# Optimization experiments

Hardware: AMD Instinct MI355X
Metric: run time of the kernel (lower is better)

## Reference

```python
import jax, jax.numpy as jnp
import numpy as np

D_MODEL = 2048
N_HEADS = 32
N_KV = 8
HEAD_DIM = D_MODEL // N_HEADS  # 64
ROPE_BASE = 500000.0


def _rope_tables(seq_len, dim, dtype):
    inv_freq = 1.0 / (ROPE_BASE ** (jnp.arange(0, dim, 2, dtype=jnp.float32) / dim))
    t = jnp.arange(seq_len, dtype=jnp.float32)
    freqs = jnp.outer(t, inv_freq)          # [S, dim/2]
    emb = jnp.concatenate([freqs, freqs], axis=-1)  # [S, dim]
    return jnp.cos(emb).astype(dtype), jnp.sin(emb).astype(dtype)


def _rotate_half(x):
    x1, x2 = jnp.split(x, 2, axis=-1)
    return jnp.concatenate([-x2, x1], axis=-1)


def setup_inputs() -> dict:
    key = jax.random.key(0)
    ks = jax.random.split(key, 5)
    B, S = 2, 2048
    sc = 0.02
    return {
        "x": jax.random.normal(ks[0], (B, S, D_MODEL), jnp.float32),
        "Wq": jax.random.normal(ks[1], (D_MODEL, N_HEADS * HEAD_DIM), jnp.float32) * sc,
        "Wk": jax.random.normal(ks[2], (D_MODEL, N_KV * HEAD_DIM), jnp.float32) * sc,
        "Wv": jax.random.normal(ks[3], (D_MODEL, N_KV * HEAD_DIM), jnp.float32) * sc,
        "Wo": jax.random.normal(ks[4], (N_HEADS * HEAD_DIM, D_MODEL), jnp.float32) * sc,
    }


def reference(x, Wq, Wk, Wv, Wo):
    B, S, _ = x.shape
    n_rep = N_HEADS // N_KV

    q = (x @ Wq).reshape(B, S, N_HEADS, HEAD_DIM)
    k = (x @ Wk).reshape(B, S, N_KV, HEAD_DIM)
    v = (x @ Wv).reshape(B, S, N_KV, HEAD_DIM)

    cos, sin = _rope_tables(S, HEAD_DIM, x.dtype)
    cos = cos[None, :, None, :]  # [1,S,1,D]
    sin = sin[None, :, None, :]
    q = q * cos + _rotate_half(q) * sin
    k = k * cos + _rotate_half(k) * sin

    # GQA without materializing expanded K/V: group q heads by kv head.
    qg = q.reshape(B, S, N_KV, n_rep, HEAD_DIM)
    scale = 1.0 / jnp.sqrt(jnp.asarray(HEAD_DIM, x.dtype))
    # scores: [B, n_kv, n_rep, Sq, Sk]
    scores = jnp.einsum("bqhrd,bkhd->bhrqk", qg, k) * scale
    attn = jax.nn.softmax(scores, axis=-1)
    out = jnp.einsum("bhrqk,bkhd->bqhrd", attn, v)  # [B,S,n_kv,n_rep,D]
    out = out.reshape(B, S, N_HEADS * HEAD_DIM)
    return out @ Wo
```

## Files before the change

kernel.cpp:

```cpp
#include <hip/hip_runtime.h>
#include <hip/hip_bf16.h>
#include <stdint.h>

#define SS    2048
#define BB    2
#define MT    4096
#define DM    2048
#define NQKVC 3072

typedef __attribute__((ext_vector_type(8))) short s16x8;
typedef __attribute__((ext_vector_type(4))) short s16x4;
typedef __attribute__((ext_vector_type(4))) float f32x4;
typedef __attribute__((ext_vector_type(2))) unsigned u32x2;

typedef __attribute__((address_space(1))) const void* as1cv;
typedef __attribute__((address_space(3))) void* as3v;

__device__ __forceinline__ float b2f(int u) {
  union { unsigned u; float f; } x; x.u = ((unsigned)(u & 0xFFFF)) << 16; return x.f;
}
__device__ __forceinline__ short f2b(float f) {
  union { float f; unsigned u; } x; x.f = f;
  unsigned r = x.u + 0x7FFFu + ((x.u >> 16) & 1u);
  return (short)(r >> 16);
}
__device__ __forceinline__ void gld16(const void* g, void* l) {
  __builtin_amdgcn_global_load_lds((as1cv)(uintptr_t)g, (as3v)(uint32_t)(uintptr_t)l, 16, 0, 0);
}
__device__ __forceinline__ s16x8 ldsfrag(const char* tile, int r, int cb) {
  return *(const s16x8*)(tile + r * 128 + (cb ^ ((r & 7) << 4)));
}
__device__ __forceinline__ f32x4 mfma16(s16x8 a, s16x8 b, f32x4 c) {
  return __builtin_amdgcn_mfma_f32_16x16x32_bf16(a, b, c, 0, 0, 0);
}
__device__ __forceinline__ void swz8(int& bx, int& by) {
  int gx = gridDim.x;
  int lin = by * gx + bx;
  int tot = gx * gridDim.y;
  int s = (lin & 7) * (tot >> 3) + (lin >> 3);
  bx = s % gx;
  by = s / gx;
}

__global__ __launch_bounds__(256) void k_wpre(const float* __restrict__ x,
                                              const float* __restrict__ Wq,
                                              const float* __restrict__ Wk,
                                              const float* __restrict__ Wv,
                                              const float* __restrict__ Wo,
                                              ushort* __restrict__ xb,
                                              ushort* __restrict__ Wqkvt,
                                              ushort* __restrict__ Wot,
                                              float* __restrict__ rtab) {
  __shared__ float t[32][33];
  int bid = blockIdx.x;
  if (bid < 8192) {
    int i = (bid * 256 + threadIdx.x) * 4;
    float4 v = *(const float4*)(x + i);
    s16x4 o = { f2b(v.x), f2b(v.y), f2b(v.z), f2b(v.w) };
    *(s16x4*)(xb + i) = o;
    return;
  }
  bid -= 8192;
  if (bid >= 10240) {
    int idx = (bid - 10240) * 256 + threadIdx.x;
    int d = idx & 31, s = idx >> 5;
    float invf = exp2f(-(float)d * (18.931568569324174f / 32.0f));
    float sn, c;
    sincosf((float)s * invf, &sn, &c);
    rtab[idx * 2]     = c;
    rtab[idx * 2 + 1] = sn;
    return;
  }
  const float* W; ushort* out; int N; int l;
  if (bid < 4096)      { W = Wq; out = Wqkvt;                         N = 2048; l = bid; }
  else if (bid < 5120) { W = Wk; out = Wqkvt + (size_t)2048 * 2048;   N = 512;  l = bid - 4096; }
  else if (bid < 6144) { W = Wv; out = Wqkvt + (size_t)2560 * 2048;   N = 512;  l = bid - 5120; }
  else                 { W = Wo; out = Wot;                           N = 2048; l = bid - 6144; }
  int k0 = (l & 63) * 32, n0 = (l >> 6) * 32;
  int tx = threadIdx.x & 31, ty = threadIdx.x >> 5;
#pragma unroll
  for (int j = 0; j < 32; j += 8)
    t[ty + j][tx] = W[(size_t)(k0 + ty + j) * N + n0 + tx];
  __syncthreads();
  int tx2 = threadIdx.x & 15, rr = threadIdx.x >> 4;
#pragma unroll
  for (int j = 0; j < 32; j += 16) {
    int nl = rr + j;
    ushort2 w;
    w.x = (ushort)f2b(t[tx2 * 2][nl]);
    w.y = (ushort)f2b(t[tx2 * 2 + 1][nl]);
    *(ushort2*)(out + (size_t)(n0 + nl) * 2048 + k0 + tx2 * 2) = w;
  }
}

template <int BF16_OUT, int ROPE>
__global__ __launch_bounds__(256) void k_gemm(const ushort* __restrict__ A,
                                              const ushort* __restrict__ B,
                                              void* __restrict__ Cv,
                                              const float* __restrict__ rtab,
                                              ushort* __restrict__ Vt,
                                              int M, int N, int K) {
  __shared__ __align__(16) char lds[32768];
  char* ldsA = lds;
  char* ldsB = lds + 16384;
  int bx = blockIdx.x, by = blockIdx.y;
  swz8(bx, by);
  int tid = threadIdx.x, lane = tid & 63, wid = tid >> 6;
  int wr = wid >> 1, wc = wid & 1;
  int row0 = by * 128, col0 = bx * 128;
  int fr = lane & 15, fq = lane >> 4;
  f32x4 acc[4][4] = {};
  int rl = lane >> 3;
  int cbs = ((lane & 7) << 4) ^ (rl << 4);
  const char* Ab = (const char*)A;
  const char* Bb = (const char*)B;
  size_t ldb = (size_t)K * 2;

  for (int kt = 0; kt < K; kt += 64) {
#pragma unroll
    for (int i = 0; i < 4; i++) {
      int ra = wid * 32 + i * 8 + rl;
      gld16(Ab + (size_t)(row0 + ra) * ldb + (size_t)kt * 2 + cbs,
            ldsA + (wid * 32 + i * 8) * 128);
      gld16(Bb + (size_t)(col0 + ra) * ldb + (size_t)kt * 2 + cbs,
            ldsB + (wid * 32 + i * 8) * 128);
    }
    __syncthreads();
#pragma unroll
    for (int kk = 0; kk < 2; kk++) {
      int cb = kk * 64 + (fq << 4);
      s16x8 af[4], bg[4];
#pragma unroll
      for (int m = 0; m < 4; m++) af[m] = ldsfrag(ldsA, wr * 64 + m * 16 + fr, cb);
#pragma unroll
      for (int n = 0; n < 4; n++) bg[n] = ldsfrag(ldsB, wc * 64 + n * 16 + fr, cb);
#pragma unroll
      for (int m = 0; m < 4; m++)
#pragma unroll
        for (int n = 0; n < 4; n++)
          acc[m][n] = mfma16(af[m], bg[n], acc[m][n]);
    }
    __syncthreads();
  }

  int cb0 = col0 + wc * 64;

  if (ROPE && col0 >= 2560) {
    __syncthreads();
    char* tw = lds + wid * 8192;
#pragma unroll
    for (int m = 0; m < 4; m++)
#pragma unroll
      for (int n = 0; n < 4; n++) {
        int cl = n * 16 + fr;
        unsigned u01, u23;
        asm("v_cvt_pk_bf16_f32 %0, %1, %2" : "=v"(u01) : "v"(acc[m][n][0]), "v"(acc[m][n][1]));
        asm("v_cvt_pk_bf16_f32 %0, %1, %2" : "=v"(u23) : "v"(acc[m][n][2]), "v"(acc[m][n][3]));
        u32x2 w = {u01, u23};
        *(u32x2*)(tw + cl * 128 + (((m * 16 + fq * 4) * 2) ^ ((cl & 7) << 4))) = w;
      }
    asm volatile("" ::: "memory");
    int b = row0 >> 11;
    int s0 = row0 - b * 2048 + wr * 64;
    int vrow0 = b * 512 + (cb0 - 2560);
#pragma unroll
    for (int jj = 0; jj < 8; jj++) {
      int cl = jj * 8 + (lane >> 3);
      int ch = lane & 7;
      s16x8 v = *(const s16x8*)(tw + cl * 128 + ((ch * 16) ^ ((cl & 7) << 4)));
      *(s16x8*)(Vt + (size_t)(vrow0 + cl) * SS + s0 + ch * 8) = v;
    }
    return;
  }

  if (ROPE) {
    if (cb0 < 2560) {
      float qs = (cb0 < 2048) ? 0.18033688011112042f : 1.0f;
#pragma unroll
      for (int m = 0; m < 4; m++)
#pragma unroll
        for (int i = 0; i < 4; i++) {
          int srow = (row0 + wr * 64 + m * 16 + fq * 4 + i) & (SS - 1);
          const float* tr = rtab + srow * 64;
          float cs0 = tr[fr * 2],        sn0 = tr[fr * 2 + 1];
          float cs1 = tr[32 + fr * 2],   sn1 = tr[32 + fr * 2 + 1];
          float lo0 = acc[m][0][i], hi0 = acc[m][2][i];
          acc[m][0][i] = (lo0 * cs0 - hi0 * sn0) * qs;
          acc[m][2][i] = (hi0 * cs0 + lo0 * sn0) * qs;
          float lo1 = acc[m][1][i], hi1 = acc[m][3][i];
          acc[m][1][i] = (lo1 * cs1 - hi1 * sn1) * qs;
          acc[m][3][i] = (hi1 * cs1 + lo1 * sn1) * qs;
        }
    }
  }

#pragma unroll
  for (int m = 0; m < 4; m++) {
#pragma unroll
    for (int i = 0; i < 4; i++) {
      int row = row0 + wr * 64 + m * 16 + fq * 4 + i;
      if (BF16_OUT) {
        ushort* C = (ushort*)Cv;
#pragma unroll
        for (int n = 0; n < 4; n++)
          C[(size_t)row * N + col0 + wc * 64 + n * 16 + fr] = (ushort)f2b(acc[m][n][i]);
      } else {
        float* C = (float*)Cv;
#pragma unroll
        for (int n = 0; n < 4; n++)
          C[(size_t)row * N + col0 + wc * 64 + n * 16 + fr] = acc[m][n][i];
      }
    }
  }
}

__global__ __launch_bounds__(256) void k_attn(const ushort* __restrict__ QKV,
                                              const ushort* __restrict__ Vt,
                                              ushort* __restrict__ O) {
  __shared__ __align__(16) char ldsK[16384];
  __shared__ __align__(16) char ldsV[16384];
  __shared__ __align__(16) char ldsP[4][2048];
  int bx = blockIdx.x, by = blockIdx.y;
  swz8(bx, by);
  int tid = threadIdx.x, lane = tid & 63, wid = tid >> 6;
  int bh = by, b = bh >> 5, h = bh & 31, kv = h >> 2;
  int fr = lane & 15, fq = lane >> 4;
  int q0 = bx * 128 + wid * 32;

  s16x8 qf[2][2];
#pragma unroll
  for (int kk = 0; kk < 2; kk++)
#pragma unroll
    for (int qi = 0; qi < 2; qi++)
      qf[kk][qi] = *(const s16x8*)(QKV + (size_t)(b * SS + q0 + qi * 16 + fr) * NQKVC
                                   + h * 64 + kk * 32 + fq * 8);

  const f32x4 fz = {0.f, 0.f, 0.f, 0.f};
  f32x4 o[4][2];
  f32x4 psum[2] = {fz, fz};
#pragma unroll
  for (int n = 0; n < 4; n++) { o[n][0] = fz; o[n][1] = fz; }
  const short ONE = 0x3F80;
  const s16x8 ones = {ONE, ONE, ONE, ONE, ONE, ONE, ONE, ONE};

  int rl = lane >> 3;
  int cbs = ((lane & 7) << 4) ^ (rl << 4);
  const char* Kbase = (const char*)QKV + (size_t)(b * SS) * (NQKVC * 2) + (size_t)(2048 + kv * 64) * 2;
  const char* Vbase = (const char*)Vt + (size_t)((b * 8 + kv) * 64) * (SS * 2);
  char* pw = ldsP[wid];
  int pswz = (fr & 7) << 4;

  for (int t = 0; t < SS / 128; t++) {
#pragma unroll
    for (int j = 0; j < 4; j++) {
      int rr = wid * 32 + j * 8;
      gld16(Kbase + (size_t)(t * 128 + rr + rl) * (NQKVC * 2) + cbs, ldsK + rr * 128);
    }
#pragma unroll
    for (int hh = 0; hh < 2; hh++)
#pragma unroll
      for (int j = 0; j < 2; j++) {
        int rr = wid * 16 + j * 8;
        gld16(Vbase + (size_t)(rr + rl) * (SS * 2) + (size_t)t * 256 + hh * 128 + cbs,
              ldsV + (hh * 64 + rr) * 128);
      }
    __syncthreads();

#pragma unroll
    for (int hh = 0; hh < 2; hh++) {
      const char* Kc = ldsK + hh * 8192;
      const char* Vc = ldsV + hh * 8192;

      f32x4 sf[4][2];
#pragma unroll
      for (int n = 0; n < 4; n++) { sf[n][0] = fz; sf[n][1] = fz; }
#pragma unroll
      for (int kk = 0; kk < 2; kk++) {
        int cb = kk * 64 + (fq << 4);
#pragma unroll
        for (int n = 0; n < 4; n++) {
          s16x8 kf = ldsfrag(Kc, n * 16 + fr, cb);
          sf[n][0] = mfma16(kf, qf[kk][0], sf[n][0]);
          sf[n][1] = mfma16(kf, qf[kk][1], sf[n][1]);
        }
      }

#pragma unroll
      for (int qi = 0; qi < 2; qi++) {
        char* pwr = pw + fr * 128;
#pragma unroll
        for (int n = 0; n < 4; n++) {
          float e0 = __builtin_amdgcn_exp2f(sf[n][qi][0]);
          float e1 = __builtin_amdgcn_exp2f(sf[n][qi][1]);
          float e2 = __builtin_amdgcn_exp2f(sf[n][qi][2]);
          float e3 = __builtin_amdgcn_exp2f(sf[n][qi][3]);
          unsigned u01, u23;
          asm("v_cvt_pk_bf16_f32 %0, %1, %2" : "=v"(u01) : "v"(e0), "v"(e1));
          asm("v_cvt_pk_bf16_f32 %0, %1, %2" : "=v"(u23) : "v"(e2), "v"(e3));
          u32x2 w = {u01, u23};
          *(u32x2*)(pwr + ((n * 32 + fq * 8) ^ pswz)) = w;
        }
        asm volatile("" ::: "memory");
#pragma unroll
        for (int kk = 0; kk < 2; kk++) {
          int cb = kk * 64 + (fq << 4);
          s16x8 pa = ldsfrag(pw, fr, cb);
          psum[qi] = mfma16(pa, ones, psum[qi]);
#pragma unroll
          for (int n = 0; n < 4; n++) {
            s16x8 vf = ldsfrag(Vc, n * 16 + fr, cb);
            o[n][qi] = mfma16(pa, vf, o[n][qi]);
          }
        }
        asm volatile("" ::: "memory");
      }
    }
    __syncthreads();
  }

#pragma unroll
  for (int qi = 0; qi < 2; qi++) {
    float inv[4];
#pragma unroll
    for (int i = 0; i < 4; i++) inv[i] = 1.0f / psum[qi][i];
#pragma unroll
    for (int n = 0; n < 4; n++) {
      float e0 = o[n][qi][0] * inv[0], e1 = o[n][qi][1] * inv[1];
      float e2 = o[n][qi][2] * inv[2], e3 = o[n][qi][3] * inv[3];
      unsigned u01, u23;
      asm("v_cvt_pk_bf16_f32 %0, %1, %2" : "=v"(u01) : "v"(e0), "v"(e1));
      asm("v_cvt_pk_bf16_f32 %0, %1, %2" : "=v"(u23) : "v"(e2), "v"(e3));
      int colb = n * 32 + fr * 2;
#pragma unroll
      for (int i = 0; i < 4; i++) {
        int r = fq * 4 + i;
        unsigned v16 = (i == 0) ? (u01 & 0xffffu) : (i == 1) ? (u01 >> 16)
                      : (i == 2) ? (u23 & 0xffffu) : (u23 >> 16);
        *(short*)(pw + r * 128 + (colb ^ ((r & 7) << 4))) = (short)v16;
      }
    }
    asm volatile("" ::: "memory");
    int orow = lane >> 2;
    int cbase = (lane & 3) * 32;
    int swo = (orow & 7) << 4;
    s16x8 ov0 = *(const s16x8*)(pw + orow * 128 + (cbase ^ swo));
    s16x8 ov1 = *(const s16x8*)(pw + orow * 128 + ((cbase + 16) ^ swo));
    ushort* dst = O + (size_t)(b * SS + bx * 128 + wid * 32 + qi * 16 + orow) * DM + h * 64 + (lane & 3) * 16;
    *(s16x8*)(dst)     = ov0;
    *(s16x8*)(dst + 8) = ov1;
    asm volatile("" ::: "memory");
  }
}

extern "C" void kernel_launch(void* const* d_in, const int* in_sizes, int n_in,
                              void* d_out, int out_size, void* d_ws, size_t ws_size,
                              hipStream_t stream) {
  const float* x  = (const float*)d_in[0];
  const float* Wq = (const float*)d_in[1];
  const float* Wk = (const float*)d_in[2];
  const float* Wv = (const float*)d_in[3];
  const float* Wo = (const float*)d_in[4];
  char* ws = (char*)d_ws;
  ushort* xb    = (ushort*)(ws);
  ushort* Wqkvt = (ushort*)(ws + 16777216);
  ushort* Wot   = (ushort*)(ws + 29360128);
  ushort* QKV   = (ushort*)(ws + 37748736);
  ushort* Vt    = (ushort*)(ws + 62914560);
  ushort* Obuf  = (ushort*)(ws + 67108864);
  float* rtab = (ws_size >= (size_t)83886080 + 524288)
              ? (float*)(ws + 83886080) : (float*)d_out;

  k_wpre<<<18688, 256, 0, stream>>>(x, Wq, Wk, Wv, Wo, xb, Wqkvt, Wot, rtab);
  k_gemm<1, 1><<<dim3(24, 32), 256, 0, stream>>>(xb, Wqkvt, (void*)QKV, rtab, Vt, MT, NQKVC, DM);
  k_attn<<<dim3(16, 64), 256, 0, stream>>>(QKV, Vt, Obuf);
  k_gemm<0, 0><<<dim3(16, 32), 256, 0, stream>>>(Obuf, Wot, d_out, nullptr, nullptr, MT, DM, DM);
}
```

Baseline: 239.0 us.

## Read V fragments directly from global memory instead of staging in LDS

The attention kernel stops staging the transposed V tile in shared memory; each wave loads its V fragments straight from global (L2-resident) memory. The P buffer is doubled so both query sub-tiles are written before a single PV loop that reuses each V fragment for two MFMAs, and launch bounds request 4 blocks per CU. This cuts LDS footprint and LDS traffic to raise occupancy, at the cost of redundant uncoalesced global reads of V per wave and more exposed global latency inside the inner loop.

Result: slower. 286.7 us (+20.0%).

```diff
diff --git a/kernel.cpp b/kernel.cpp
--- a/kernel.cpp
+++ b/kernel.cpp
@@ -214,12 +214,11 @@
   }
 }
 
-__global__ __launch_bounds__(256) void k_attn(const ushort* __restrict__ QKV,
-                                              const ushort* __restrict__ Vt,
-                                              ushort* __restrict__ O) {
+__global__ __launch_bounds__(256, 4) void k_attn(const ushort* __restrict__ QKV,
+                                                 const ushort* __restrict__ Vt,
+                                                 ushort* __restrict__ O) {
   __shared__ __align__(16) char ldsK[16384];
-  __shared__ __align__(16) char ldsV[16384];
-  __shared__ __align__(16) char ldsP[4][2048];
+  __shared__ __align__(16) char ldsP[4][4096];
   int bx = blockIdx.x, by = blockIdx.y;
   swz8(bx, by);
   int tid = threadIdx.x, lane = tid & 63, wid = tid >> 6;
@@ -246,7 +245,7 @@
   int rl = lane >> 3;
   int cbs = ((lane & 7) << 4) ^ (rl << 4);
   const char* Kbase = (const char*)QKV + (size_t)(b * SS) * (NQKVC * 2) + (size_t)(2048 + kv * 64) * 2;
-  const char* Vbase = (const char*)Vt + (size_t)((b * 8 + kv) * 64) * (SS * 2);
+  const ushort* Vg = Vt + (size_t)((b * 8 + kv) * 64) * SS;
   char* pw = ldsP[wid];
   int pswz = (fr & 7) << 4;
 
@@ -256,20 +255,12 @@
       int rr = wid * 32 + j * 8;
       gld16(Kbase + (size_t)(t * 128 + rr + rl) * (NQKVC * 2) + cbs, ldsK + rr * 128);
     }
-#pragma unroll
-    for (int hh = 0; hh < 2; hh++)
-#pragma unroll
-      for (int j = 0; j < 2; j++) {
-        int rr = wid * 16 + j * 8;
-        gld16(Vbase + (size_t)(rr + rl) * (SS * 2) + (size_t)t * 256 + hh * 128 + cbs,
-              ldsV + (hh * 64 + rr) * 128);
-      }
     __syncthreads();
 
 #pragma unroll
     for (int hh = 0; hh < 2; hh++) {
       const char* Kc = ldsK + hh * 8192;
-      const char* Vc = ldsV + hh * 8192;
+      int sbase = t * 128 + hh * 64;
 
       f32x4 sf[4][2];
 #pragma unroll
@@ -287,7 +278,7 @@
 
 #pragma unroll
       for (int qi = 0; qi < 2; qi++) {
-        char* pwr = pw + fr * 128;
+        char* pwr = pw + qi * 2048 + fr * 128;
 #pragma unroll
         for (int n = 0; n < 4; n++) {
           float e0 = __builtin_amdgcn_exp2f(sf[n][qi][0]);
@@ -300,20 +291,27 @@
           u32x2 w = {u01, u23};
           *(u32x2*)(pwr + ((n * 32 + fq * 8) ^ pswz)) = w;
         }
-        asm volatile("" ::: "memory");
-#pragma unroll
-        for (int kk = 0; kk < 2; kk++) {
-          int cb = kk * 64 + (fq << 4);
-          s16x8 pa = ldsfrag(pw, fr, cb);
-          psum[qi] = mfma16(pa, ones, psum[qi]);
-#pragma unroll
-          for (int n = 0; n < 4; n++) {
-            s16x8 vf = ldsfrag(Vc, n * 16 + fr, cb);
-            o[n][qi] = mfma16(pa, vf, o[n][qi]);
-          }
-        }
-        asm volatile("" ::: "memory");
-      }
+      }
+      asm volatile("" ::: "memory");
+
+#pragma unroll
+      for (int kk = 0; kk < 2; kk++) {
+        int cb = kk * 64 + (fq << 4);
+        int sc = sbase + kk * 32 + fq * 8;
+        s16x8 vf0 = *(const s16x8*)(Vg + (size_t)(0 * 16 + fr) * SS + sc);
+        s16x8 vf1 = *(const s16x8*)(Vg + (size_t)(1 * 16 + fr) * SS + sc);
+        s16x8 vf2 = *(const s16x8*)(Vg + (size_t)(2 * 16 + fr) * SS + sc);
+        s16x8 vf3 = *(const s16x8*)(Vg + (size_t)(3 * 16 + fr) * SS + sc);
+        s16x8 pa0 = ldsfrag(pw, fr, cb);
+        s16x8 pa1 = ldsfrag(pw + 2048, fr, cb);
+        psum[0] = mfma16(pa0, ones, psum[0]);
+        psum[1] = mfma16(pa1, ones, psum[1]);
+        o[0][0] = mfma16(pa0, vf0, o[0][0]);  o[0][1] = mfma16(pa1, vf0, o[0][1]);
+        o[1][0] = mfma16(pa0, vf1, o[1][0]);  o[1][1] = mfma16(pa1, vf1, o[1][1]);
+        o[2][0] = mfma16(pa0, vf2, o[2][0]);  o[2][1] = mfma16(pa1, vf2, o[2][1]);
+        o[3][0] = mfma16(pa0, vf3, o[3][0]);  o[3][1] = mfma16(pa1, vf3, o[3][1]);
+      }
+      asm volatile("" ::: "memory");
     }
     __syncthreads();
   }
```
